# Kernel tuning notes

Hardware: AMD Instinct MI355X
Metric: run time of the kernel (lower is better)

The kernel has to match this reference:

```python
import jax, jax.numpy as jnp
import numpy as np

N_RAYS = 1_048_576
T_ITERS = 4
N_POINTS = 8
DIM = 64
N_LAYERS = 2
INF = 1e9


def setup_inputs() -> dict:
    key = jax.random.key(0)
    ks = jax.random.split(key, 12)
    orig = jax.random.normal(ks[0], (N_RAYS, 3), jnp.float32)
    vec = jax.random.normal(ks[1], (N_RAYS, 3), jnp.float32)
    masks = jax.random.bernoulli(ks[2], 0.6, (T_ITERS, N_RAYS))
    bbox_idxs = jax.random.randint(ks[3], (T_ITERS, N_RAYS), 0, 1024, jnp.int32)
    t1 = jax.random.uniform(ks[4], (T_ITERS, N_RAYS), jnp.float32) * 2.0
    t2 = t1 + jax.random.uniform(ks[5], (T_ITERS, N_RAYS), jnp.float32) * 2.0
    mesh_min = jnp.array([-1.0, -1.0, -1.0], jnp.float32)
    mesh_max = jnp.array([1.0, 1.0, 1.0], jnp.float32)
    s = 0.05
    W0 = jax.random.normal(ks[6], (3 * N_POINTS, DIM), jnp.float32) * s
    b0 = jnp.zeros((DIM,), jnp.float32)
    ln_g = jnp.ones((N_LAYERS, DIM), jnp.float32)
    ln_b = jnp.zeros((N_LAYERS, DIM), jnp.float32)
    Ws = jax.random.normal(ks[7], (N_LAYERS, DIM, DIM), jnp.float32) * s
    bs = jnp.zeros((N_LAYERS, DIM), jnp.float32)
    Wc = jax.random.normal(ks[8], (DIM,), jnp.float32) * s
    bc = jnp.zeros((), jnp.float32)
    Wd = jax.random.normal(ks[9], (DIM,), jnp.float32) * s
    bd = jnp.zeros((), jnp.float32)
    return dict(orig=orig, vec=vec, masks=masks, bbox_idxs=bbox_idxs, t1=t1, t2=t2,
                mesh_min=mesh_min, mesh_max=mesh_max, W0=W0, b0=b0,
                ln_g=ln_g, ln_b=ln_b, Ws=Ws, bs=bs, Wc=Wc, bc=bc, Wd=Wd, bd=bd)


def _layernorm(x, g, b):
    mu = jnp.mean(x, axis=-1, keepdims=True)
    var = jnp.mean((x - mu) ** 2, axis=-1, keepdims=True)
    return (x - mu) * jax.lax.rsqrt(var + 1e-5) * g + b


def _net_forward(x, W0, b0, ln_g, ln_b, Ws, bs, Wc, bc, Wd, bd):
    # x: [N, 3*n_points]
    y = x @ W0 + b0
    for i in range(N_LAYERS):
        y = jax.nn.relu(y)
        y = _layernorm(y, ln_g[i], ln_b[i])
        y = y @ Ws[i] + bs[i]
    y = jax.nn.relu(y)
    cls = y @ Wc + bc   # [N]
    dist = y @ Wd + bd  # [N]
    return cls, dist


def reference(orig, vec, masks, bbox_idxs, t1, t2, mesh_min, mesh_max,
              W0, b0, ln_g, ln_b, Ws, bs, Wc, bc, Wd, bd):
    n_rays = orig.shape[0]
    ts = jnp.linspace(0.0, 1.0, N_POINTS, dtype=jnp.float32)
    min_infl = mesh_min - 0.5 * (mesh_max - mesh_min)
    max_infl = mesh_max + 0.5 * (mesh_max - mesh_min)
    scale = max_infl - min_infl
    dist = jnp.full((n_rays,), INF, jnp.float32)
    for it in range(T_ITERS):
        mask, ct1, ct2 = masks[it], t1[it], t2[it]
        inp_orig = orig + vec * ct1[:, None]          # [N,3]
        inp_vec = vec * (ct2 - ct1)[:, None]          # [N,3]
        # sample n_points along segment: [N, P, 3]
        inp = inp_orig[:, None, :] + inp_vec[:, None, :] * ts[None, :, None]
        inp = (inp - min_infl) / scale
        x = inp.reshape(n_rays, -1)                   # [N, 3P]
        hit_c, dv_c = _net_forward(x, W0, b0, ln_g, ln_b, Ws, bs, Wc, bc, Wd, bd)
        hit = jnp.where(mask, hit_c, 0.0)             # masked_scatter_ equivalent
        dv = jnp.where(mask, dv_c, 0.0) + ct1
        upd = (hit > 0) & (dv < dist) & mask
        dist = jnp.where(upd, dv, dist)
    dist = jnp.where(dist == INF, 0.0, dist)
    return (dist > 0, dist)
```

## Files before the change

kernel.cpp:

```cpp
#include <hip/hip_runtime.h>
#include <hip/hip_bf16.h>
#include <stdint.h>

#define NRAYS 1048576
#define INFV  1e9f
#define TBIG  1e30f

typedef short short8 __attribute__((ext_vector_type(8)));
typedef float f32x4  __attribute__((ext_vector_type(4)));

#define WS_B0   16
#define FB0     1024
#define FB1     2048

#define PKLO(a,b) ((int)(((unsigned)(a) & 0xFFFFu) | ((unsigned)(b) << 16)))
#define PKHI(a,b) ((int)(((unsigned)(a) >> 16) | ((unsigned)(b) & 0xFFFF0000u)))

__device__ __forceinline__ float ldf(const void* p, int i, int fm) {
    if (fm) return ((const float*)p)[i];
    unsigned u = ((const unsigned short*)p)[i];
    return __uint_as_float(u << 16);
}

__device__ __forceinline__ void split3(float f, int& him, int& lo) {
    unsigned u = __float_as_uint(f);
    float r = f - __uint_as_float(u & 0xFFFF0000u);
    unsigned um = __float_as_uint(r);
    float r2 = r - __uint_as_float(um & 0xFFFF0000u);
    unsigned ul = __float_as_uint(r2);
    him = (int)((u >> 16) | (um & 0xFFFF0000u));
    lo  = (int)(ul >> 16);
}

__device__ __forceinline__ unsigned comp16(int h, float f) {
    unsigned u = __float_as_uint(f);
    if (h == 0) return u >> 16;
    float r = f - __uint_as_float(u & 0xFFFF0000u);
    unsigned um = __float_as_uint(r);
    if (h == 1) return um >> 16;
    float r2 = r - __uint_as_float(um & 0xFFFF0000u);
    return __float_as_uint(r2) >> 16;
}

__device__ __forceinline__ float rsum16(float x) {
    int v;
    v = __builtin_amdgcn_update_dpp(0, __float_as_int(x), 0x128, 0xF, 0xF, false); x += __int_as_float(v);
    v = __builtin_amdgcn_update_dpp(0, __float_as_int(x), 0x124, 0xF, 0xF, false); x += __int_as_float(v);
    v = __builtin_amdgcn_update_dpp(0, __float_as_int(x), 0x122, 0xF, 0xF, false); x += __int_as_float(v);
    v = __builtin_amdgcn_update_dpp(0, __float_as_int(x), 0x121, 0xF, 0xF, false); x += __int_as_float(v);
    return x;
}

union I4S8 { int4 i; short8 s; };
__device__ __forceinline__ short8 mk8i(int a, int b, int c, int d) {
    I4S8 u; u.i = make_int4(a, b, c, d); return u.s;
}
__device__ __forceinline__ short8 ld_frag(const unsigned* p) {
    I4S8 u; u.i = *(const int4*)p; return u.s;
}

#define WSYNC() asm volatile("s_waitcnt lgkmcnt(0)" ::: "memory")

__global__ __launch_bounds__(256) void conv_k(
    const void* __restrict__ mmin, const void* __restrict__ mmax,
    const void* __restrict__ masks,
    const void* __restrict__ W0, const void* __restrict__ b0,
    const void* __restrict__ lng, const void* __restrict__ lnb,
    const void* __restrict__ Ws, const void* __restrict__ bs,
    const void* __restrict__ Wc, const void* __restrict__ bc,
    const void* __restrict__ Wd, const void* __restrict__ bd,
    unsigned* __restrict__ ws)
{
    __shared__ int sfm;
    float* wf = (float*)ws;
    const int tid = threadIdx.x;
    if (tid == 0) {
        unsigned w0 = ((const unsigned*)mmin)[0];
        int fm = ((w0 & 0xFFFFu) == 0u) ? 1 : 0;
        const unsigned* mw = (const unsigned*)masks;
        bool sawBf = false, allBin = true, sawF32 = false;
        for (int i = 0; i < 64; ++i) {
            unsigned w = mw[i], lo = w & 0xFFFFu, hi = w >> 16;
            if (lo == 0x3F80u && (hi == 0x3F80u || hi == 0u)) sawBf = true;
            if (w == 0x3F800000u) sawF32 = true;
            if (w > 1u) allBin = false;
        }
        int ms = sawBf ? 2 : (allBin ? 4 : (sawF32 ? 4 : 1));
        ws[8] = (unsigned)fm; ws[9] = (unsigned)ms;
        for (int c = 0; c < 3; ++c) {
            float mn = ldf(mmin, c, fm), mx = ldf(mmax, c, fm);
            float ext = mx - mn;
            wf[c]     = mn - 0.5f * ext;
            wf[3 + c] = 1.0f / (2.0f * ext);
        }
        wf[6] = ldf(bc, 0, fm);
        wf[7] = ldf(bd, 0, fm);
        sfm = fm;
    }
    __syncthreads();
    const int fm = sfm;

    for (int i = tid; i < 64;  i += 256) { wf[16 + i] = ldf(b0, i, fm); wf[464 + i] = ldf(Wc, i, fm); wf[528 + i] = ldf(Wd, i, fm); }
    for (int i = tid; i < 128; i += 256) { wf[80 + i] = ldf(bs, i, fm); wf[208 + i] = ldf(lng, i, fm); wf[336 + i] = ldf(lnb, i, fm); }

    for (int w = tid; w < 768; w += 256) {
        int ct = w / 192, rem = w % 192;
        int h = rem / 64, wi = rem % 64;
        int lane16 = wi >> 2, p = wi & 3;
        int n = ct * 16 + lane16;
        unsigned word = 0;
        #pragma unroll
        for (int half = 0; half < 2; ++half) {
            int k = 2 * p + half;
            float v = 0.f;
            if (k < 3) {
                for (int pp = 0; pp < 8; ++pp) v += ldf(W0, (3 * pp + k) * 64 + n, fm);
            } else if (k < 6) {
                int c3 = k - 3;
                for (int pp = 0; pp < 8; ++pp) v = fmaf((float)((double)pp / 7.0), ldf(W0, (3 * pp + c3) * 64 + n, fm), v);
            }
            word |= comp16(h, v) << (16 * half);
        }
        ws[FB0 + ((ct * 3 + h) * 16 + lane16) * 4 + p] = word;
    }

    for (int w = tid; w < 12288; w += 256) {
        int li = w / 6144, inner = w % 6144;
        int t = inner >> 8;
        int h = t % 3, ckc = t / 3, kc = ckc & 1, ct = ckc >> 1;
        int wi = inner & 255, lane = wi >> 2, p = wi & 3;
        int qq = lane >> 4, cc = lane & 15;
        int n = ct * 16 + cc;
        int k0 = kc * 32 + qq * 8 + 2 * p;
        float f0 = ldf(Ws, li * 4096 + k0 * 64 + n, fm);
        float f1 = ldf(Ws, li * 4096 + (k0 + 1) * 64 + n, fm);
        ws[FB1 + w] = comp16(h, f0) | (comp16(h, f1) << 16);
    }
}

#define ST1_S 34
#define ST2_S 34

__global__ __launch_bounds__(128, 4) void nbvh_main(
    const void* __restrict__ orig_p, const void* __restrict__ vec_p,
    const void* __restrict__ masks_p, const void* __restrict__ t1_p,
    const void* __restrict__ t2_p, const unsigned* __restrict__ wsu,
    void* __restrict__ out_p)
{
    __shared__ __align__(16) unsigned sT1[2][16][ST1_S];
    __shared__ __align__(16) unsigned sT2[2][16][ST2_S];
    __shared__ float sOV[2][6][64];
    __shared__ float sT1m[2][4][64];
    __shared__ float sT2g[2][4][64];
    __shared__ float sDf[2][64];

    const float* wf = (const float*)wsu;
    const int fm = (int)wsu[8];
    const int ms = (int)wsu[9];
    const float bcv = wf[6], bdv = wf[7];

    const int tid = threadIdx.x;
    const int Wv  = tid >> 6;
    const int L   = tid & 63;
    const int q = L >> 4, c = L & 15;
    const int ray = blockIdx.x * 128 + tid;

    unsigned (&T1)[16][ST1_S] = sT1[Wv];
    unsigned (&T2)[16][ST2_S] = sT2[Wv];
    float (&OV)[6][64]  = sOV[Wv];
    float (&T1m)[4][64] = sT1m[Wv];
    float (&T2g)[4][64] = sT2g[Wv];
    float (&Df)[64]     = sDf[Wv];

    {
        const float mn0 = wf[0], mn1 = wf[1], mn2 = wf[2];
        const float is0 = wf[3], is1 = wf[4], is2 = wf[5];
        const float o0 = ldf(orig_p, 3*ray+0, fm), o1 = ldf(orig_p, 3*ray+1, fm), o2 = ldf(orig_p, 3*ray+2, fm);
        const float v0 = ldf(vec_p,  3*ray+0, fm), v1 = ldf(vec_p,  3*ray+1, fm), v2 = ldf(vec_p,  3*ray+2, fm);
        OV[0][L] = (o0 - mn0) * is0;  OV[1][L] = (o1 - mn1) * is1;  OV[2][L] = (o2 - mn2) * is2;
        OV[3][L] = v0 * is0;          OV[4][L] = v1 * is1;          OV[5][L] = v2 * is2;
        #pragma unroll
        for (int it = 0; it < 4; ++it) {
            const int gi = it * NRAYS + ray;
            bool mk;
            if      (ms == 1) mk = ((const uint8_t*) masks_p)[gi] != 0;
            else if (ms == 2) mk = ((const uint16_t*)masks_p)[gi] != 0;
            else              mk = ((const unsigned*) masks_p)[gi] != 0;
            T1m[it][L] = mk ? ldf(t1_p, gi, fm) : TBIG;
            T2g[it][L] = ldf(t2_p, gi, fm);
        }
        Df[L] = INFV;
    }
    WSYNC();

    float b0r[4], wcr[4], wdr[4];
    #pragma unroll
    for (int ct = 0; ct < 4; ++ct) {
        b0r[ct] = wf[16  + ct * 16 + c];
        wcr[ct] = wf[464 + ct * 16 + c];
        wdr[ct] = wf[528 + ct * 16 + c];
    }

    #pragma unroll 1
    for (int rt = 0; rt < 4; ++rt) {
        #pragma unroll 1
        for (int ip = 0; ip < 2; ++ip) {
            f32x4 acc[2][4];
            short8 Ah[2][2], Am[2][2], Al[2][2];

            {
                short8 Xh[2], Xm[2], Xl[2];
                #pragma unroll
                for (int itl = 0; itl < 2; ++itl) {
                    const int it = ip * 2 + itl;
                    const int row = rt * 16 + c;
                    const float t1v = T1m[it][row];
                    const float dtv = T2g[it][row] - t1v;
                    float x[6];
                    #pragma unroll
                    for (int j = 0; j < 3; ++j) {
                        float ov = OV[j][row], vv = OV[3 + j][row];
                        x[j]     = fmaf(vv, t1v, ov);
                        x[3 + j] = vv * dtv;
                    }
                    int him[6], lo[6];
                    #pragma unroll
                    for (int j = 0; j < 6; ++j) split3(q == 0 ? x[j] : 0.f, him[j], lo[j]);
                    Xh[itl] = mk8i(PKLO(him[0],him[1]), PKLO(him[2],him[3]), PKLO(him[4],him[5]), 0);
                    Xm[itl] = mk8i(PKHI(him[0],him[1]), PKHI(him[2],him[3]), PKHI(him[4],him[5]), 0);
                    Xl[itl] = mk8i(PKLO(lo[0], lo[1]),  PKLO(lo[2], lo[3]),  PKLO(lo[4], lo[5]),  0);
                }
                #pragma unroll
                for (int itl = 0; itl < 2; ++itl)
                    #pragma unroll
                    for (int ct = 0; ct < 4; ++ct) {
                        float b = b0r[ct];
                        f32x4 a; a[0]=a[1]=a[2]=a[3]=b; acc[itl][ct]=a;
                    }
                #pragma unroll
                for (int ct = 0; ct < 4; ++ct) {
                    short8 Bh = (q==0) ? ld_frag(wsu + FB0 + ((ct*3+0)*16 + c)*4) : mk8i(0,0,0,0);
                    short8 Bm = (q==0) ? ld_frag(wsu + FB0 + ((ct*3+1)*16 + c)*4) : mk8i(0,0,0,0);
                    short8 Bl = (q==0) ? ld_frag(wsu + FB0 + ((ct*3+2)*16 + c)*4) : mk8i(0,0,0,0);
                    #pragma unroll
                    for (int itl = 0; itl < 2; ++itl) {
                        acc[itl][ct] = __builtin_amdgcn_mfma_f32_16x16x32_bf16(Xh[itl], Bh, acc[itl][ct], 0,0,0);
                        acc[itl][ct] = __builtin_amdgcn_mfma_f32_16x16x32_bf16(Xh[itl], Bm, acc[itl][ct], 0,0,0);
                        acc[itl][ct] = __builtin_amdgcn_mfma_f32_16x16x32_bf16(Xm[itl], Bh, acc[itl][ct], 0,0,0);
                        acc[itl][ct] = __builtin_amdgcn_mfma_f32_16x16x32_bf16(Xm[itl], Bm, acc[itl][ct], 0,0,0);
                        acc[itl][ct] = __builtin_amdgcn_mfma_f32_16x16x32_bf16(Xh[itl], Bl, acc[itl][ct], 0,0,0);
                        acc[itl][ct] = __builtin_amdgcn_mfma_f32_16x16x32_bf16(Xl[itl], Bh, acc[itl][ct], 0,0,0);
                    }
                }
            }

            #pragma unroll 1
            for (int layer = 0; layer < 2; ++layer) {
                const unsigned* fb = wsu + FB1 + layer * 6144;
                const int bo = 80 + layer * 64, go = 208 + layer * 64, ho = 336 + layer * 64;

                float gvr[4], hvr[4], bvr[4];
                #pragma unroll
                for (int ct = 0; ct < 4; ++ct) {
                    gvr[ct] = wf[go + ct * 16 + c];
                    hvr[ct] = wf[ho + ct * 16 + c];
                    bvr[ct] = wf[bo + ct * 16 + c];
                }

                #pragma unroll
                for (int itl = 0; itl < 2; ++itl) {
                    WSYNC();
                    float z[4][4];
                    #pragma unroll
                    for (int ct = 0; ct < 4; ++ct)
                        #pragma unroll
                        for (int e = 0; e < 4; ++e) z[ct][e] = fmaxf(acc[itl][ct][e], 0.f);
                    float mu[4], rs[4];
                    #pragma unroll
                    for (int e = 0; e < 4; ++e) {
                        float s  = z[0][e] + z[1][e] + z[2][e] + z[3][e];
                        float s2 = fmaf(z[0][e], z[0][e], fmaf(z[1][e], z[1][e],
                                   fmaf(z[2][e], z[2][e], z[3][e] * z[3][e])));
                        s  = rsum16(s);
                        s2 = rsum16(s2);
                        mu[e] = s * (1.0f / 64.0f);
                        float var = fmaf(-mu[e], mu[e], s2 * (1.0f / 64.0f));
                        rs[e] = rsqrtf(var + 1e-5f);
                    }
                    int him[4][4], lov[4][4];
                    #pragma unroll
                    for (int ct = 0; ct < 4; ++ct) {
                        const float gv = gvr[ct];
                        const float hv = hvr[ct];
                        #pragma unroll
                        for (int e = 0; e < 4; ++e) {
                            float y = fmaf((z[ct][e] - mu[e]) * rs[e], gv, hv);
                            split3(y, him[ct][e], lov[ct][e]);
                        }
                    }
                    #pragma unroll
                    for (int e = 0; e < 4; ++e) {
                        const int row = q * 4 + e;
                        T1[row][c]      = (unsigned)him[0][e];
                        T1[row][c + 16] = (unsigned)him[1][e];
                        T2[row][c]      = (unsigned)PKLO(lov[0][e], lov[2][e]);
                        T2[row][c + 16] = (unsigned)PKLO(lov[1][e], lov[3][e]);
                    }
                    WSYNC();
                    const int4 t01 = *(const int4*)&T2[c][q*8];
                    const int4 t23 = *(const int4*)&T2[c][q*8 + 4];
                    {
                        const int4 w01 = *(const int4*)&T1[c][q*8];
                        const int4 w23 = *(const int4*)&T1[c][q*8 + 4];
                        Ah[itl][0] = mk8i(PKLO(w01.x,w01.y), PKLO(w01.z,w01.w), PKLO(w23.x,w23.y), PKLO(w23.z,w23.w));
                        Am[itl][0] = mk8i(PKHI(w01.x,w01.y), PKHI(w01.z,w01.w), PKHI(w23.x,w23.y), PKHI(w23.z,w23.w));
                        Al[itl][0] = mk8i(PKLO(t01.x,t01.y), PKLO(t01.z,t01.w), PKLO(t23.x,t23.y), PKLO(t23.z,t23.w));
                    }
                    WSYNC();
                    #pragma unroll
                    for (int e = 0; e < 4; ++e) {
                        const int row = q * 4 + e;
                        T1[row][c]      = (unsigned)him[2][e];
                        T1[row][c + 16] = (unsigned)him[3][e];
                    }
                    WSYNC();
                    {
                        const int4 w01 = *(const int4*)&T1[c][q*8];
                        const int4 w23 = *(const int4*)&T1[c][q*8 + 4];
                        Ah[itl][1] = mk8i(PKLO(w01.x,w01.y), PKLO(w01.z,w01.w), PKLO(w23.x,w23.y), PKLO(w23.z,w23.w));
                        Am[itl][1] = mk8i(PKHI(w01.x,w01.y), PKHI(w01.z,w01.w), PKHI(w23.x,w23.y), PKHI(w23.z,w23.w));
                        Al[itl][1] = mk8i(PKHI(t01.x,t01.y), PKHI(t01.z,t01.w), PKHI(t23.x,t23.y), PKHI(t23.z,t23.w));
                    }
                }

                #pragma unroll
                for (int itl = 0; itl < 2; ++itl)
                    #pragma unroll
                    for (int ct = 0; ct < 4; ++ct) {
                        float b = bvr[ct];
                        f32x4 a; a[0]=a[1]=a[2]=a[3]=b; acc[itl][ct]=a;
                    }
                #pragma unroll
                for (int kc = 0; kc < 2; ++kc) {
                    #pragma unroll
                    for (int ct = 0; ct < 4; ++ct) {
                        short8 Bh = ld_frag(fb + (((ct*2+kc)*3 + 0) << 8) + (L << 2));
                        short8 Bm = ld_frag(fb + (((ct*2+kc)*3 + 1) << 8) + (L << 2));
                        short8 Bl = ld_frag(fb + (((ct*2+kc)*3 + 2) << 8) + (L << 2));
                        #pragma unroll
                        for (int itl = 0; itl < 2; ++itl) {
                            acc[itl][ct] = __builtin_amdgcn_mfma_f32_16x16x32_bf16(Ah[itl][kc], Bh, acc[itl][ct], 0,0,0);
                            acc[itl][ct] = __builtin_amdgcn_mfma_f32_16x16x32_bf16(Ah[itl][kc], Bm, acc[itl][ct], 0,0,0);
                            acc[itl][ct] = __builtin_amdgcn_mfma_f32_16x16x32_bf16(Am[itl][kc], Bh, acc[itl][ct], 0,0,0);
                            acc[itl][ct] = __builtin_amdgcn_mfma_f32_16x16x32_bf16(Am[itl][kc], Bm, acc[itl][ct], 0,0,0);
                            acc[itl][ct] = __builtin_amdgcn_mfma_f32_16x16x32_bf16(Ah[itl][kc], Bl, acc[itl][ct], 0,0,0);
                            acc[itl][ct] = __builtin_amdgcn_mfma_f32_16x16x32_bf16(Al[itl][kc], Bh, acc[itl][ct], 0,0,0);
                        }
                    }
                }
            }

            {
                #pragma unroll
                for (int e = 0; e < 4; ++e) {
                    const int idx = rt * 16 + q * 4 + e;
                    float d = Df[idx];
                    #pragma unroll
                    for (int itl = 0; itl < 2; ++itl) {
                        const int it = ip * 2 + itl;
                        float cp = 0.f, dp = 0.f;
                        #pragma unroll
                        for (int ct = 0; ct < 4; ++ct) {
                            float f = fmaxf(acc[itl][ct][e], 0.f);
                            cp = fmaf(f, wcr[ct], cp);
                            dp = fmaf(f, wdr[ct], dp);
                        }
                        cp = rsum16(cp); dp = rsum16(dp);
                        float cls = cp + bcv;
                        float dv  = dp + bdv + T1m[it][idx];
                        if (cls > 0.f && dv < d) d = dv;
                    }
                    if (c == 0) Df[idx] = d;
                }
            }
        }
    }

    WSYNC();
    float d = Df[L];
    if (d == INFV) d = 0.f;
    const float hit = (d > 0.f) ? 1.f : 0.f;
    if (fm) {
        ((float*)out_p)[ray]         = hit;
        ((float*)out_p)[NRAYS + ray] = d;
    } else {
        __hip_bfloat16* o = (__hip_bfloat16*)out_p;
        o[ray]         = __float2bfloat16(hit);
        o[NRAYS + ray] = __float2bfloat16(d);
    }
}

extern "C" void kernel_launch(void* const* d_in, const int* in_sizes, int n_in,
                              void* d_out, int out_size, void* d_ws, size_t ws_size,
                              hipStream_t stream) {
    (void)in_sizes; (void)n_in; (void)ws_size; (void)out_size;
    unsigned* ws = (unsigned*)d_ws;
    conv_k<<<1, 256, 0, stream>>>(
        d_in[6], d_in[7], d_in[2],
        d_in[8], d_in[9], d_in[10], d_in[11],
        d_in[12], d_in[13], d_in[14], d_in[15],
        d_in[16], d_in[17], ws);
    nbvh_main<<<NRAYS / 128, 128, 0, stream>>>(
        d_in[0], d_in[1], d_in[2], d_in[4], d_in[5], ws, d_out);
}
```

Measured before the change: 836.3 us.

## Fold LayerNorm affine into weights, use perm packing, drop occupancy hint, add setprio

Folds the LayerNorm gamma into the per-layer weight matrices and beta into the biases during preprocessing, removing the per-element affine step from the main loop. It replaces shift/mask packing of bf16 splits with v_perm byte-permute intrinsics and drops the q==0 zeroing in the input split. It also removes the minimum-blocks launch bound, moves per-thread weight/bias register loads into the loops to ease register pressure, and wraps the MFMA blocks with s_setprio. Folding changes rounding slightly, and removing the occupancy hint may change register allocation and occupancy.

```diff
diff --git a/kernel.cpp b/kernel.cpp
--- a/kernel.cpp
+++ b/kernel.cpp
@@ -15,6 +15,13 @@
 
 #define PKLO(a,b) ((int)(((unsigned)(a) & 0xFFFFu) | ((unsigned)(b) << 16)))
 #define PKHI(a,b) ((int)(((unsigned)(a) >> 16) | ((unsigned)(b) & 0xFFFF0000u)))
+
+__device__ __forceinline__ int pklo(int a, int b) {
+    return (int)__builtin_amdgcn_perm((unsigned)b, (unsigned)a, 0x05040100u);
+}
+__device__ __forceinline__ int pkhi(int a, int b) {
+    return (int)__builtin_amdgcn_perm((unsigned)b, (unsigned)a, 0x07060302u);
+}
 
 __device__ __forceinline__ float ldf(const void* p, int i, int fm) {
     if (fm) return ((const float*)p)[i];
@@ -22,14 +29,13 @@
     return __uint_as_float(u << 16);
 }
 
-__device__ __forceinline__ void split3(float f, int& him, int& lo) {
+__device__ __forceinline__ void split3(float f, int& him, int& lo_raw) {
     unsigned u = __float_as_uint(f);
     float r = f - __uint_as_float(u & 0xFFFF0000u);
     unsigned um = __float_as_uint(r);
     float r2 = r - __uint_as_float(um & 0xFFFF0000u);
-    unsigned ul = __float_as_uint(r2);
-    him = (int)((u >> 16) | (um & 0xFFFF0000u));
-    lo  = (int)(ul >> 16);
+    him    = pkhi((int)u, (int)um);
+    lo_raw = (int)__float_as_uint(r2);
 }
 
 __device__ __forceinline__ unsigned comp16(int h, float f) {
@@ -101,7 +107,13 @@
     const int fm = sfm;
 
     for (int i = tid; i < 64;  i += 256) { wf[16 + i] = ldf(b0, i, fm); wf[464 + i] = ldf(Wc, i, fm); wf[528 + i] = ldf(Wd, i, fm); }
-    for (int i = tid; i < 128; i += 256) { wf[80 + i] = ldf(bs, i, fm); wf[208 + i] = ldf(lng, i, fm); wf[336 + i] = ldf(lnb, i, fm); }
+    for (int i = tid; i < 128; i += 256) {
+        int li = i >> 6, n = i & 63;
+        float b = ldf(bs, i, fm);
+        for (int k = 0; k < 64; ++k)
+            b = fmaf(ldf(lnb, li * 64 + k, fm), ldf(Ws, li * 4096 + k * 64 + n, fm), b);
+        wf[80 + i] = b;
+    }
 
     for (int w = tid; w < 768; w += 256) {
         int ct = w / 192, rem = w % 192;
@@ -132,8 +144,10 @@
         int qq = lane >> 4, cc = lane & 15;
         int n = ct * 16 + cc;
         int k0 = kc * 32 + qq * 8 + 2 * p;
-        float f0 = ldf(Ws, li * 4096 + k0 * 64 + n, fm);
-        float f1 = ldf(Ws, li * 4096 + (k0 + 1) * 64 + n, fm);
+        float g0 = ldf(lng, li * 64 + k0, fm);
+        float g1 = ldf(lng, li * 64 + k0 + 1, fm);
+        float f0 = g0 * ldf(Ws, li * 4096 + k0 * 64 + n, fm);
+        float f1 = g1 * ldf(Ws, li * 4096 + (k0 + 1) * 64 + n, fm);
         ws[FB1 + w] = comp16(h, f0) | (comp16(h, f1) << 16);
     }
 }
@@ -141,7 +155,7 @@
 #define ST1_S 34
 #define ST2_S 34
 
-__global__ __launch_bounds__(128, 4) void nbvh_main(
+__global__ __launch_bounds__(128) void nbvh_main(
     const void* __restrict__ orig_p, const void* __restrict__ vec_p,
     const void* __restrict__ masks_p, const void* __restrict__ t1_p,
     const void* __restrict__ t2_p, const unsigned* __restrict__ wsu,
@@ -193,14 +207,6 @@
     }
     WSYNC();
 
-    float b0r[4], wcr[4], wdr[4];
-    #pragma unroll
-    for (int ct = 0; ct < 4; ++ct) {
-        b0r[ct] = wf[16  + ct * 16 + c];
-        wcr[ct] = wf[464 + ct * 16 + c];
-        wdr[ct] = wf[528 + ct * 16 + c];
-    }
-
     #pragma unroll 1
     for (int rt = 0; rt < 4; ++rt) {
         #pragma unroll 1
@@ -225,18 +231,19 @@
                     }
                     int him[6], lo[6];
                     #pragma unroll
-                    for (int j = 0; j < 6; ++j) split3(q == 0 ? x[j] : 0.f, him[j], lo[j]);
-                    Xh[itl] = mk8i(PKLO(him[0],him[1]), PKLO(him[2],him[3]), PKLO(him[4],him[5]), 0);
-                    Xm[itl] = mk8i(PKHI(him[0],him[1]), PKHI(him[2],him[3]), PKHI(him[4],him[5]), 0);
-                    Xl[itl] = mk8i(PKLO(lo[0], lo[1]),  PKLO(lo[2], lo[3]),  PKLO(lo[4], lo[5]),  0);
+                    for (int j = 0; j < 6; ++j) split3(x[j], him[j], lo[j]);
+                    Xh[itl] = mk8i(pklo(him[0],him[1]), pklo(him[2],him[3]), pklo(him[4],him[5]), 0);
+                    Xm[itl] = mk8i(pkhi(him[0],him[1]), pkhi(him[2],him[3]), pkhi(him[4],him[5]), 0);
+                    Xl[itl] = mk8i(pkhi(lo[0], lo[1]),  pkhi(lo[2], lo[3]),  pkhi(lo[4], lo[5]),  0);
                 }
                 #pragma unroll
                 for (int itl = 0; itl < 2; ++itl)
                     #pragma unroll
                     for (int ct = 0; ct < 4; ++ct) {
-                        float b = b0r[ct];
+                        float b = wf[16 + ct * 16 + c];
                         f32x4 a; a[0]=a[1]=a[2]=a[3]=b; acc[itl][ct]=a;
                     }
+                __builtin_amdgcn_s_setprio(1);
                 #pragma unroll
                 for (int ct = 0; ct < 4; ++ct) {
                     short8 Bh = (q==0) ? ld_frag(wsu + FB0 + ((ct*3+0)*16 + c)*4) : mk8i(0,0,0,0);
@@ -252,20 +259,12 @@
                         acc[itl][ct] = __builtin_amdgcn_mfma_f32_16x16x32_bf16(Xl[itl], Bh, acc[itl][ct], 0,0,0);
                     }
                 }
+                __builtin_amdgcn_s_setprio(0);
             }
 
             #pragma unroll 1
             for (int layer = 0; layer < 2; ++layer) {
                 const unsigned* fb = wsu + FB1 + layer * 6144;
-                const int bo = 80 + layer * 64, go = 208 + layer * 64, ho = 336 + layer * 64;
-
-                float gvr[4], hvr[4], bvr[4];
-                #pragma unroll
-                for (int ct = 0; ct < 4; ++ct) {
-                    gvr[ct] = wf[go + ct * 16 + c];
-                    hvr[ct] = wf[ho + ct * 16 + c];
-                    bvr[ct] = wf[bo + ct * 16 + c];
-                }
 
                 #pragma unroll
                 for (int itl = 0; itl < 2; ++itl) {
@@ -290,11 +289,9 @@
                     int him[4][4], lov[4][4];
                     #pragma unroll
                     for (int ct = 0; ct < 4; ++ct) {
-                        const float gv = gvr[ct];
-                        const float hv = hvr[ct];
                         #pragma unroll
                         for (int e = 0; e < 4; ++e) {
-                            float y = fmaf((z[ct][e] - mu[e]) * rs[e], gv, hv);
+                            float y = (z[ct][e] - mu[e]) * rs[e];
                             split3(y, him[ct][e], lov[ct][e]);
                         }
                     }
@@ -303,8 +300,8 @@
                         const int row = q * 4 + e;
                         T1[row][c]      = (unsigned)him[0][e];
                         T1[row][c + 16] = (unsigned)him[1][e];
-                        T2[row][c]      = (unsigned)PKLO(lov[0][e], lov[2][e]);
-                        T2[row][c + 16] = (unsigned)PKLO(lov[1][e], lov[3][e]);
+                        T2[row][c]      = (unsigned)pkhi(lov[0][e], lov[2][e]);
+                        T2[row][c + 16] = (unsigned)pkhi(lov[1][e], lov[3][e]);
                     }
                     WSYNC();
                     const int4 t01 = *(const int4*)&T2[c][q*8];
@@ -312,9 +309,9 @@
                     {
                         const int4 w01 = *(const int4*)&T1[c][q*8];
                         const int4 w23 = *(const int4*)&T1[c][q*8 + 4];
-                        Ah[itl][0] = mk8i(PKLO(w01.x,w01.y), PKLO(w01.z,w01.w), PKLO(w23.x,w23.y), PKLO(w23.z,w23.w));
-                        Am[itl][0] = mk8i(PKHI(w01.x,w01.y), PKHI(w01.z,w01.w), PKHI(w23.x,w23.y), PKHI(w23.z,w23.w));
-                        Al[itl][0] = mk8i(PKLO(t01.x,t01.y), PKLO(t01.z,t01.w), PKLO(t23.x,t23.y), PKLO(t23.z,t23.w));
+                        Ah[itl][0] = mk8i(pklo(w01.x,w01.y), pklo(w01.z,w01.w), pklo(w23.x,w23.y), pklo(w23.z,w23.w));
+                        Am[itl][0] = mk8i(pkhi(w01.x,w01.y), pkhi(w01.z,w01.w), pkhi(w23.x,w23.y), pkhi(w23.z,w23.w));
+                        Al[itl][0] = mk8i(pklo(t01.x,t01.y), pklo(t01.z,t01.w), pklo(t23.x,t23.y), pklo(t23.z,t23.w));
                     }
                     WSYNC();
                     #pragma unroll
@@ -327,9 +324,9 @@
                     {
                         const int4 w01 = *(const int4*)&T1[c][q*8];
                         const int4 w23 = *(const int4*)&T1[c][q*8 + 4];
-                        Ah[itl][1] = mk8i(PKLO(w01.x,w01.y), PKLO(w01.z,w01.w), PKLO(w23.x,w23.y), PKLO(w23.z,w23.w));
-                        Am[itl][1] = mk8i(PKHI(w01.x,w01.y), PKHI(w01.z,w01.w), PKHI(w23.x,w23.y), PKHI(w23.z,w23.w));
-                        Al[itl][1] = mk8i(PKHI(t01.x,t01.y), PKHI(t01.z,t01.w), PKHI(t23.x,t23.y), PKHI(t23.z,t23.w));
+                        Ah[itl][1] = mk8i(pklo(w01.x,w01.y), pklo(w01.z,w01.w), pklo(w23.x,w23.y), pklo(w23.z,w23.w));
+                        Am[itl][1] = mk8i(pkhi(w01.x,w01.y), pkhi(w01.z,w01.w), pkhi(w23.x,w23.y), pkhi(w23.z,w23.w));
+                        Al[itl][1] = mk8i(pkhi(t01.x,t01.y), pkhi(t01.z,t01.w), pkhi(t23.x,t23.y), pkhi(t23.z,t23.w));
                     }
                 }
 
@@ -337,9 +334,10 @@
                 for (int itl = 0; itl < 2; ++itl)
                     #pragma unroll
                     for (int ct = 0; ct < 4; ++ct) {
-                        float b = bvr[ct];
+                        float b = wf[80 + layer * 64 + ct * 16 + c];
                         f32x4 a; a[0]=a[1]=a[2]=a[3]=b; acc[itl][ct]=a;
                     }
+                __builtin_amdgcn_s_setprio(1);
                 #pragma unroll
                 for (int kc = 0; kc < 2; ++kc) {
                     #pragma unroll
@@ -358,9 +356,16 @@
                         }
                     }
                 }
+                __builtin_amdgcn_s_setprio(0);
             }
 
             {
+                float wcr[4], wdr[4];
+                #pragma unroll
+                for (int ct = 0; ct < 4; ++ct) {
+                    wcr[ct] = wf[464 + ct * 16 + c];
+                    wdr[ct] = wf[528 + ct * 16 + c];
+                }
                 #pragma unroll
                 for (int e = 0; e < 4; ++e) {
                     const int idx = rt * 16 + q * 4 + e;
```

Result: faster. 784.7 us (-6.2%).
